# Kernel tuning notes

Measured on AMD Instinct MI355X. Metric: run time of the kernel, lower is better.

## Reference

```python
import jax, jax.numpy as jnp
import numpy as np

N_U, N_I, E = 100000, 100000, 600000
F_U, F_I, H, OUT = 96, 160, 128, 64
EPS = 1e-5


def _params(key):
    ks = jax.random.split(key, 20)
    n = lambda i, s: (jax.random.normal(ks[i], s, jnp.float32) * 0.05)
    p = {
        # lazy per-type input projections
        'Wp_u': n(0, (F_U, H)), 'bp_u': jnp.zeros((H,), jnp.float32),
        'Wp_i': n(1, (F_I, H)), 'bp_i': jnp.zeros((H,), jnp.float32),
        # layer 0 SAGE (in=H, out=H): lin_l (neighbors, bias), lin_r (root, no bias)
        'Wl0_ui': n(2, (H, H)), 'bl0_ui': jnp.zeros((H,), jnp.float32), 'Wr0_ui': n(3, (H, H)),
        'Wl0_iu': n(4, (H, H)), 'bl0_iu': jnp.zeros((H,), jnp.float32), 'Wr0_iu': n(5, (H, H)),
        'g0_u': jnp.ones((H,), jnp.float32), 'b0_u': jnp.zeros((H,), jnp.float32),
        'g0_i': jnp.ones((H,), jnp.float32), 'b0_i': jnp.zeros((H,), jnp.float32),
        # layer 1 SAGE (in=H, out=OUT)
        'Wl1_ui': n(6, (H, OUT)), 'bl1_ui': jnp.zeros((OUT,), jnp.float32), 'Wr1_ui': n(7, (H, OUT)),
        'Wl1_iu': n(8, (H, OUT)), 'bl1_iu': jnp.zeros((OUT,), jnp.float32), 'Wr1_iu': n(9, (H, OUT)),
        'g1_u': jnp.ones((OUT,), jnp.float32), 'b1_u': jnp.zeros((OUT,), jnp.float32),
        'g1_i': jnp.ones((OUT,), jnp.float32), 'b1_i': jnp.zeros((OUT,), jnp.float32),
    }
    return p


def setup_inputs() -> dict:
    key = jax.random.key(0)
    k0, k1, k2, k3, kp = jax.random.split(key, 5)
    inp = {
        'x_user': jax.random.normal(k0, (N_U, F_U), jnp.float32),
        'x_item': jax.random.normal(k1, (N_I, F_I), jnp.float32),
        'edge_ui': jax.random.randint(k2, (2, E), 0, N_U),  # row0: src user idx, row1: dst item idx
        'edge_iu': jax.random.randint(k3, (2, E), 0, N_I),  # row0: src item idx, row1: dst user idx
    }
    inp.update(_params(kp))
    return inp


def _seg_mean(x_src, src, dst, n_dst):
    # gather source features [E, C], scatter-mean into destinations [n_dst, C]
    msg = x_src[src]
    s = jax.ops.segment_sum(msg, dst, num_segments=n_dst)
    cnt = jax.ops.segment_sum(jnp.ones((dst.shape[0], 1), x_src.dtype), dst, num_segments=n_dst)
    return s / jnp.maximum(cnt, 1.0)


def _sage(x_src, x_dst, edge, Wl, bl, Wr, n_dst):
    agg = _seg_mean(x_src, edge[0], edge[1], n_dst)
    return agg @ Wl + bl + x_dst @ Wr


def _ln(h, g, b):
    m = jnp.mean(h, axis=-1, keepdims=True)
    v = jnp.mean(jnp.square(h - m), axis=-1, keepdims=True)
    return (h - m) * jax.lax.rsqrt(v + EPS) * g + b


def reference(x_user, x_item, edge_ui, edge_iu,
              Wp_u, bp_u, Wp_i, bp_i,
              Wl0_ui, bl0_ui, Wr0_ui, Wl0_iu, bl0_iu, Wr0_iu,
              g0_u, b0_u, g0_i, b0_i,
              Wl1_ui, bl1_ui, Wr1_ui, Wl1_iu, bl1_iu, Wr1_iu,
              g1_u, b1_u, g1_i, b1_i):
    # per-type input projection + ReLU
    h_u = jax.nn.relu(x_user @ Wp_u + bp_u)
    h_i = jax.nn.relu(x_item @ Wp_i + bp_i)
    # layer 0: HeteroConv(sum) of SAGEConv per edge type, then per-type LN + ReLU (dropout = eval identity)
    h_i1 = _sage(h_u, h_i, edge_ui, Wl0_ui, bl0_ui, Wr0_ui, N_I)
    h_u1 = _sage(h_i, h_u, edge_iu, Wl0_iu, bl0_iu, Wr0_iu, N_U)
    h_u1 = jax.nn.relu(_ln(h_u1, g0_u, b0_u))
    h_i1 = jax.nn.relu(_ln(h_i1, g0_i, b0_i))
    # layer 1 (final): SAGE -> LN, no ReLU/dropout
    h_i2 = _sage(h_u1, h_i1, edge_ui, Wl1_ui, bl1_ui, Wr1_ui, N_I)
    h_u2 = _sage(h_i1, h_u1, edge_iu, Wl1_iu, bl1_iu, Wr1_iu, N_U)
    h_u2 = _ln(h_u2, g1_u, b1_u)
    h_i2 = _ln(h_i2, g1_i, b1_i)
    return h_u2, h_i2
```

## Files before the change

kernel.cpp:

```cpp
#include <hip/hip_runtime.h>

typedef __attribute__((ext_vector_type(8))) __bf16 bf16x8;
typedef __attribute__((ext_vector_type(4))) float floatx4;
typedef __attribute__((ext_vector_type(8))) unsigned short ushort8v;
typedef __attribute__((ext_vector_type(4))) unsigned short ushort4v;

namespace {
constexpr int kNU = 100000, kNI = 100000, kE = 600000;
constexpr int kFU = 96, kFI = 160, kH = 128, kOUT = 64;
constexpr float kEPS = 1e-5f;
constexpr int kM = 32;
constexpr int kNCHUNK = 98;
constexpr int kNBLK = kNU / kM;
constexpr int kEB = (kE + 255) / 256;
constexpr int kPART = kNU / 8;
}

__device__ __forceinline__ unsigned short f2b(float f) {
  unsigned u = __builtin_bit_cast(unsigned, f);
  u += 0x7FFFu + ((u >> 16) & 1u);
  return (unsigned short)(u >> 16);
}
__device__ __forceinline__ float b2f(unsigned short h) {
  return __builtin_bit_cast(float, (unsigned)h << 16);
}
__device__ __forceinline__ void split3(float v, unsigned short& h,
                                       unsigned short& m, unsigned short& l) {
  h = f2b(v);
  const float r1 = v - b2f(h);
  m = f2b(r1);
  const float r2 = r1 - b2f(m);
  l = f2b(r2);
}
__device__ __forceinline__ void split2(float v, unsigned short& h,
                                       unsigned short& m) {
  h = f2b(v);
  m = f2b(v - b2f(h));
}
__device__ __forceinline__ bf16x8 ldb8(const unsigned short* p) {
  return __builtin_bit_cast(bf16x8, *(const ushort8v*)p);
}
__device__ __forceinline__ floatx4 mfma16(bf16x8 a, bf16x8 b, floatx4 c) {
  return __builtin_amdgcn_mfma_f32_16x16x32_bf16(a, b, c, 0, 0, 0);
}
__device__ __forceinline__ unsigned short* ab_ptr(unsigned short* base,
                                                  int plane, int r, int bo) {
  return (unsigned short*)((char*)base + plane * 8192 + r * 256 +
                           (bo ^ ((r & 7) << 4)));
}

struct WcvtArgs {
  const float* src[10];
  unsigned short* dh[10];
  unsigned short* dm[10];
  unsigned short* dl[10];
  int K[10], N[10];
};
__global__ __launch_bounds__(256) void wcvt(WcvtArgs a) {
  const int m = blockIdx.y;
  const int K = a.K[m], N = a.N[m];
  const int idx = blockIdx.x * 256 + threadIdx.x;
  if (idx < K * N) {
    const int n = idx / K, k = idx - n * K;
    unsigned short h, mm, l;
    split3(a.src[m][(size_t)k * N + n], h, mm, l);
    a.dh[m][idx] = h;
    a.dm[m][idx] = mm;
    a.dl[m][idx] = l;
  }
}

__global__ void zero_int(int* __restrict__ p, int n) {
  int i = blockIdx.x * blockDim.x + threadIdx.x;
  const int st = gridDim.x * blockDim.x;
  for (; i < n; i += st) p[i] = 0;
}

__global__ __launch_bounds__(1024) void scanA(const int* __restrict__ cnt_u,
                                              const int* __restrict__ cnt_i,
                                              int* ptr_u, int* ptr_i, int* tot) {
  __shared__ int sh[1024];
  const int dir = blockIdx.y;
  const int* cnt = dir ? cnt_i : cnt_u;
  int* ptr = dir ? ptr_i : ptr_u;
  const int t = threadIdx.x;
  const int i = blockIdx.x * 1024 + t;
  const int v = (i < kNU) ? cnt[i] : 0;
  sh[t] = v;
  __syncthreads();
  for (int o = 1; o < 1024; o <<= 1) {
    const int y = (t >= o) ? sh[t - o] : 0;
    __syncthreads();
    sh[t] += y;
    __syncthreads();
  }
  if (i < kNU) ptr[i] = sh[t] - v;
  if (t == 1023) tot[dir * 128 + blockIdx.x] = sh[1023];
}

__global__ __launch_bounds__(128) void scanB(int* tot) {
  __shared__ int sh[128];
  int* tp = tot + blockIdx.x * 128;
  const int t = threadIdx.x;
  const int v = (t < kNCHUNK) ? tp[t] : 0;
  sh[t] = v;
  __syncthreads();
  for (int o = 1; o < 128; o <<= 1) {
    const int y = (t >= o) ? sh[t - o] : 0;
    __syncthreads();
    sh[t] += y;
    __syncthreads();
  }
  if (t < kNCHUNK) tp[t] = sh[t] - v;
}

__global__ __launch_bounds__(1024) void scanC(int* ptr_u, int* ptr_i,
                                              const int* __restrict__ tot,
                                              int* cur_u, int* cur_i) {
  const int dir = blockIdx.y;
  int* ptr = dir ? ptr_i : ptr_u;
  int* cur = dir ? cur_i : cur_u;
  const int i = blockIdx.x * 1024 + threadIdx.x;
  if (i < kNU) {
    const int v = ptr[i] + tot[dir * 128 + blockIdx.x];
    ptr[i] = v;
    cur[i] = v;
  }
}

template <int F>
__device__ __forceinline__ void proj_body(
    const float* __restrict__ x, const unsigned short* __restrict__ Wh,
    const unsigned short* __restrict__ Wm, const unsigned short* __restrict__ Wl,
    const float* __restrict__ bias, float* __restrict__ out, int blk,
    unsigned short* sh) {
  constexpr int AS = F + 8, KC = F / 32;
  unsigned short* Ah = sh;
  unsigned short* Am = sh + kM * AS;
  unsigned short* Al = sh + 2 * kM * AS;
  const int tid = threadIdx.x;
  const size_t row0 = (size_t)blk * kM;
  for (int c = tid; c < kM * (F / 4); c += 256) {
    const int r = c / (F / 4), j = c % (F / 4);
    const float4 v = *(const float4*)&x[(row0 + r) * F + j * 4];
    const float* vv = &v.x;
    ushort4v h4, m4, l4;
#pragma unroll
    for (int u = 0; u < 4; ++u) {
      unsigned short th, tm, tl;
      split3(vv[u], th, tm, tl);
      h4[u] = th; m4[u] = tm; l4[u] = tl;
    }
    *(ushort4v*)&Ah[r * AS + j * 4] = h4;
    *(ushort4v*)&Am[r * AS + j * 4] = m4;
    *(ushort4v*)&Al[r * AS + j * 4] = l4;
  }
  const int lane = tid & 63, w = tid >> 6, q = lane >> 4, ln = lane & 15;
  floatx4 acc[2][2] = {}, accL[2][2] = {};
  __syncthreads();
#pragma unroll
  for (int kc = 0; kc < KC; ++kc) {
    bf16x8 bh[2], bm[2], bl_[2];
#pragma unroll
    for (int t = 0; t < 2; ++t) {
      const int off = (w * 32 + t * 16 + ln) * F + kc * 32 + q * 8;
      bh[t] = ldb8(&Wh[off]);
      bm[t] = ldb8(&Wm[off]);
      bl_[t] = ldb8(&Wl[off]);
    }
#pragma unroll
    for (int mt = 0; mt < 2; ++mt) {
      const int ro = mt * 16 + ln, co = kc * 32 + q * 8;
      const bf16x8 ah = ldb8(&Ah[ro * AS + co]);
      const bf16x8 am = ldb8(&Am[ro * AS + co]);
      const bf16x8 al = ldb8(&Al[ro * AS + co]);
#pragma unroll
      for (int t = 0; t < 2; ++t) {
        acc[mt][t] = mfma16(ah, bh[t], acc[mt][t]);
        floatx4 cl = accL[mt][t];
        cl = mfma16(ah, bm[t], cl);
        cl = mfma16(am, bh[t], cl);
        cl = mfma16(ah, bl_[t], cl);
        cl = mfma16(al, bh[t], cl);
        cl = mfma16(am, bm[t], cl);
        accL[mt][t] = cl;
      }
    }
  }
#pragma unroll
  for (int t = 0; t < 2; ++t) {
    const int col = w * 32 + t * 16 + ln;
    const float bv = bias[col];
#pragma unroll
    for (int mt = 0; mt < 2; ++mt)
#pragma unroll
      for (int r = 0; r < 4; ++r)
        out[(row0 + mt * 16 + q * 4 + r) * kH + col] =
            fmaxf((acc[mt][t][r] + accL[mt][t][r]) + bv, 0.f);
  }
}

__global__ __launch_bounds__(256, 4) void hist_proj(
    const int* __restrict__ eui, const int* __restrict__ eiu, int* cnt_i,
    int* cnt_u, const float* __restrict__ x,
    const unsigned short* __restrict__ Wh, const unsigned short* __restrict__ Wm,
    const unsigned short* __restrict__ Wl, const float* __restrict__ bias,
    float* __restrict__ out) {
  __shared__ __align__(16) unsigned short sh[3 * kM * (kFU + 8)];
  if (blockIdx.x < 8 * kEB) {
    const int part = blockIdx.x & 7, slice = blockIdx.x >> 3;
    const int e = slice * 256 + threadIdx.x;
    if (e < kE) {
      const int di = eui[kE + e];
      if (di / kPART == part) atomicAdd(&cnt_i[di], 1);
      const int du = eiu[kE + e];
      if (du / kPART == part) atomicAdd(&cnt_u[du], 1);
    }
  } else {
    proj_body<kFU>(x, Wh, Wm, Wl, bias, out, blockIdx.x - 8 * kEB, sh);
  }
}

__global__ __launch_bounds__(256, 4) void fill_proj(
    const int* __restrict__ eui, const int* __restrict__ eiu, int* cur_i,
    int* cur_u, int* __restrict__ col_ui, int* __restrict__ col_iu,
    const float* __restrict__ x, const unsigned short* __restrict__ Wh,
    const unsigned short* __restrict__ Wm, const unsigned short* __restrict__ Wl,
    const float* __restrict__ bias, float* __restrict__ out) {
  __shared__ __align__(16) unsigned short sh[3 * kM * (kFI + 8)];
  if (blockIdx.x < 8 * kEB) {
    const int part = blockIdx.x & 7, slice = blockIdx.x >> 3;
    const int e = slice * 256 + threadIdx.x;
    if (e < kE) {
      const int di = eui[kE + e];
      if (di / kPART == part) {
        const int p = atomicAdd(&cur_i[di], 1);
        col_ui[p] = eui[e];
      }
      const int du = eiu[kE + e];
      if (du / kPART == part) {
        const int p2 = atomicAdd(&cur_u[du], 1);
        col_iu[p2] = eiu[e];
      }
    }
  } else {
    proj_body<kFI>(x, Wh, Wm, Wl, bias, out, blockIdx.x - 8 * kEB, sh);
  }
}

struct AggArgs {
  const float* src[2];
  const int* ptr[2];
  const int* cur[2];
  const int* col[2];
  float* out[2];
};
template <int W>
__global__ __launch_bounds__(256) void agg2(AggArgs a) {
  const int dir = blockIdx.y;
  const int w = threadIdx.x >> 6, lane = threadIdx.x & 63;
  const int row = blockIdx.x * 4 + w;
  const float* __restrict__ feat = a.src[dir];
  const int* __restrict__ col = a.col[dir];
  const int beg = a.ptr[dir][row], end = a.cur[dir][row];
  const float inv = 1.0f / fmaxf((float)(end - beg), 1.0f);
  if (W == 128) {
    float s0 = 0.f, s1 = 0.f;
    for (int e = beg; e < end; e += 8) {
      const int n = end - e;
      float2 v[8];
#pragma unroll
      for (int j = 0; j < 8; ++j)
        if (j < n) v[j] = *(const float2*)&feat[(size_t)col[e + j] * 128 + lane * 2];
#pragma unroll
      for (int j = 0; j < 8; ++j)
        if (j < n) { s0 += v[j].x; s1 += v[j].y; }
    }
    float2 o;
    o.x = s0 * inv;
    o.y = s1 * inv;
    *(float2*)&a.out[dir][(size_t)row * 128 + lane * 2] = o;
  } else {
    float s = 0.f;
    for (int e = beg; e < end; e += 8) {
      const int n = end - e;
      float v[8];
#pragma unroll
      for (int j = 0; j < 8; ++j)
        if (j < n) v[j] = feat[(size_t)col[e + j] * 64 + lane];
#pragma unroll
      for (int j = 0; j < 8; ++j)
        if (j < n) s += v[j];
    }
    a.out[dir][(size_t)row * 64 + lane] = s * inv;
  }
}

struct FsArgs {
  const float* agg[2];
  const float* root[2];
  const unsigned short *WLh[2], *WLm[2];
  const unsigned short *WRh[2], *WRm[2];
  const float *bl[2], *g[2], *b[2];
  float* out[2];
};
__global__ __launch_bounds__(256, 5) void sage0(FsArgs a) {
  constexpr int NOUT = 128;
  __shared__ __align__(16) unsigned short Ab[4 * kM * kH];
  float* Cs = (float*)Ab;
  const int tid = threadIdx.x;
  const int dir = blockIdx.y;
  const size_t row0 = (size_t)blockIdx.x * kM;
  const float* __restrict__ agg = a.agg[dir];
  const float* __restrict__ root = a.root[dir];

  {
    float4 va[8];
#pragma unroll
    for (int k = 0; k < 8; ++k) {
      const int c = tid + k * 256;
      const int cc = c & 1023, r = cc >> 5, j = cc & 31;
      va[k] = *(const float4*)((k < 4 ? agg : root) + (row0 + r) * kH + j * 4);
    }
#pragma unroll
    for (int k = 0; k < 8; ++k) {
      const int c = tid + k * 256;
      const int mat = k >> 2, cc = c & 1023, r = cc >> 5, j = cc & 31;
      const float* vv = &va[k].x;
      ushort4v h4, m4;
#pragma unroll
      for (int u = 0; u < 4; ++u) {
        unsigned short th, tm;
        split2(vv[u], th, tm);
        h4[u] = th; m4[u] = tm;
      }
      *(ushort4v*)ab_ptr(Ab, mat * 2 + 0, r, j * 8) = h4;
      *(ushort4v*)ab_ptr(Ab, mat * 2 + 1, r, j * 8) = m4;
    }
  }

  const int lane = tid & 63, w = tid >> 6, q = lane >> 4, ln = lane & 15;
  floatx4 acc[2][2] = {}, accL[2][2] = {};
  const unsigned short* __restrict__ WLh = a.WLh[dir];
  const unsigned short* __restrict__ WLm = a.WLm[dir];
  const unsigned short* __restrict__ WRh = a.WRh[dir];
  const unsigned short* __restrict__ WRm = a.WRm[dir];
  __syncthreads();
#pragma unroll
  for (int kc = 0; kc < 4; ++kc) {
    bf16x8 BL[2][2], BR[2][2];
#pragma unroll
    for (int t = 0; t < 2; ++t) {
      const int off = (w * 32 + t * 16 + ln) * kH + kc * 32 + q * 8;
      BL[0][t] = ldb8(&WLh[off]);
      BL[1][t] = ldb8(&WLm[off]);
      BR[0][t] = ldb8(&WRh[off]);
      BR[1][t] = ldb8(&WRm[off]);
    }
#pragma unroll
    for (int mt = 0; mt < 2; ++mt) {
      const int ro = mt * 16 + ln, cob = kc * 64 + q * 16;
      const bf16x8 a1h = ldb8(ab_ptr(Ab, 0, ro, cob));
      const bf16x8 a1m = ldb8(ab_ptr(Ab, 1, ro, cob));
      const bf16x8 a2h = ldb8(ab_ptr(Ab, 2, ro, cob));
      const bf16x8 a2m = ldb8(ab_ptr(Ab, 3, ro, cob));
#pragma unroll
      for (int t = 0; t < 2; ++t) {
        floatx4 c = acc[mt][t];
        c = mfma16(a1h, BL[0][t], c);
        c = mfma16(a2h, BR[0][t], c);
        acc[mt][t] = c;
        floatx4 cl = accL[mt][t];
        cl = mfma16(a1h, BL[1][t], cl);
        cl = mfma16(a1m, BL[0][t], cl);
        cl = mfma16(a2h, BR[1][t], cl);
        cl = mfma16(a2m, BR[0][t], cl);
        accL[mt][t] = cl;
      }
    }
  }
  __syncthreads();
  const float* __restrict__ blv = a.bl[dir];
#pragma unroll
  for (int t = 0; t < 2; ++t) {
    const int colx = (w * 2 + t) * 16 + ln;
    const float bv = blv[colx];
#pragma unroll
    for (int mt = 0; mt < 2; ++mt)
#pragma unroll
      for (int r = 0; r < 4; ++r)
        Cs[(mt * 16 + q * 4 + r) * (NOUT + 1) + colx] =
            (acc[mt][t][r] + accL[mt][t][r]) + bv;
  }
  __syncthreads();
  const int r = tid >> 3, sub = tid & 7;
  const float* __restrict__ gg = a.g[dir];
  const float* __restrict__ bb = a.b[dir];
  float vals[16], s = 0.f;
#pragma unroll
  for (int j = 0; j < 16; ++j) {
    const float v = Cs[r * (NOUT + 1) + sub * 16 + j];
    vals[j] = v;
    s += v;
  }
#pragma unroll
  for (int o = 1; o < 8; o <<= 1) s += __shfl_xor(s, o, 64);
  const float mean = s * (1.0f / NOUT);
  float s2 = 0.f;
#pragma unroll
  for (int j = 0; j < 16; ++j) {
    const float d = vals[j] - mean;
    s2 += d * d;
  }
#pragma unroll
  for (int o = 1; o < 8; o <<= 1) s2 += __shfl_xor(s2, o, 64);
  const float rstd = rsqrtf(s2 * (1.0f / NOUT) + kEPS);
  float* op = a.out[dir] + (row0 + r) * NOUT + sub * 16;
#pragma unroll
  for (int j = 0; j < 16; j += 4) {
    float4 o4;
    float* oo = &o4.x;
#pragma unroll
    for (int jj = 0; jj < 4; ++jj)
      oo[jj] = fmaxf((vals[j + jj] - mean) * rstd * gg[sub * 16 + j + jj] +
                         bb[sub * 16 + j + jj],
                     0.f);
    *(float4*)&op[j] = o4;
  }
}

struct ZArgs {
  const float* src[2];
  const unsigned short *Bh[2], *Bm[2];
  float* out[2];
};
__global__ __launch_bounds__(256, 6) void zproj(ZArgs a) {
  __shared__ __align__(16) unsigned short Ab[2 * kM * kH];
  const int tid = threadIdx.x, dir = blockIdx.y;
  const size_t row0 = (size_t)blockIdx.x * kM;
  const float* __restrict__ src = a.src[dir];
  {
    float4 va[4];
#pragma unroll
    for (int k = 0; k < 4; ++k) {
      const int c = tid + k * 256, r = c >> 5, j = c & 31;
      va[k] = *(const float4*)&src[(row0 + r) * kH + j * 4];
    }
#pragma unroll
    for (int k = 0; k < 4; ++k) {
      const int c = tid + k * 256, r = c >> 5, j = c & 31;
      const float* vv = &va[k].x;
      ushort4v h4, m4;
#pragma unroll
      for (int u = 0; u < 4; ++u) {
        unsigned short th, tm;
        split2(vv[u], th, tm);
        h4[u] = th; m4[u] = tm;
      }
      *(ushort4v*)ab_ptr(Ab, 0, r, j * 8) = h4;
      *(ushort4v*)ab_ptr(Ab, 1, r, j * 8) = m4;
    }
  }
  const int lane = tid & 63, w = tid >> 6, q = lane >> 4, ln = lane & 15;
  const unsigned short* __restrict__ Bh = a.Bh[dir];
  const unsigned short* __restrict__ Bm = a.Bm[dir];
  floatx4 acc[2] = {}, accL[2] = {};
  __syncthreads();
#pragma unroll
  for (int kc = 0; kc < 4; ++kc) {
    const int off = (w * 16 + ln) * kH + kc * 32 + q * 8;
    const bf16x8 bh = ldb8(&Bh[off]);
    const bf16x8 bm = ldb8(&Bm[off]);
#pragma unroll
    for (int mt = 0; mt < 2; ++mt) {
      const int ro = mt * 16 + ln, cob = kc * 64 + q * 16;
      const bf16x8 ah = ldb8(ab_ptr(Ab, 0, ro, cob));
      const bf16x8 am = ldb8(ab_ptr(Ab, 1, ro, cob));
      acc[mt] = mfma16(ah, bh, acc[mt]);
      floatx4 cl = accL[mt];
      cl = mfma16(ah, bm, cl);
      cl = mfma16(am, bh, cl);
      accL[mt] = cl;
    }
  }
  float* __restrict__ out = a.out[dir];
  const int col = w * 16 + ln;
#pragma unroll
  for (int mt = 0; mt < 2; ++mt)
#pragma unroll
    for (int r = 0; r < 4; ++r)
      out[(row0 + mt * 16 + q * 4 + r) * kOUT + col] =
          acc[mt][r] + accL[mt][r];
}

struct S1Args {
  const float* root[2];
  const float* aggz[2];
  const unsigned short *Bh[2], *Bm[2];
  const float *bl[2], *g[2], *b[2];
  float* out[2];
};
__global__ __launch_bounds__(256, 6) void sage1(S1Args a) {
  constexpr int NOUT = kOUT;
  __shared__ __align__(16) unsigned short Ab[2 * kM * kH];
  float* Cs = (float*)Ab;
  const int tid = threadIdx.x, dir = blockIdx.y;
  const size_t row0 = (size_t)blockIdx.x * kM;
  const float* __restrict__ root = a.root[dir];
  {
    float4 va[4];
#pragma unroll
    for (int k = 0; k < 4; ++k) {
      const int c = tid + k * 256, r = c >> 5, j = c & 31;
      va[k] = *(const float4*)&root[(row0 + r) * kH + j * 4];
    }
#pragma unroll
    for (int k = 0; k < 4; ++k) {
      const int c = tid + k * 256, r = c >> 5, j = c & 31;
      const float* vv = &va[k].x;
      ushort4v h4, m4;
#pragma unroll
      for (int u = 0; u < 4; ++u) {
        unsigned short th, tm;
        split2(vv[u], th, tm);
        h4[u] = th; m4[u] = tm;
      }
      *(ushort4v*)ab_ptr(Ab, 0, r, j * 8) = h4;
      *(ushort4v*)ab_ptr(Ab, 1, r, j * 8) = m4;
    }
  }
  const int lane = tid & 63, w = tid >> 6, q = lane >> 4, ln = lane & 15;
  const unsigned short* __restrict__ Bh = a.Bh[dir];
  const unsigned short* __restrict__ Bm = a.Bm[dir];
  floatx4 acc[2] = {}, accL[2] = {};
  __syncthreads();
#pragma unroll
  for (int kc = 0; kc < 4; ++kc) {
    const int off = (w * 16 + ln) * kH + kc * 32 + q * 8;
    const bf16x8 bh = ldb8(&Bh[off]);
    const bf16x8 bm = ldb8(&Bm[off]);
#pragma unroll
    for (int mt = 0; mt < 2; ++mt) {
      const int ro = mt * 16 + ln, cob = kc * 64 + q * 16;
      const bf16x8 ah = ldb8(ab_ptr(Ab, 0, ro, cob));
      const bf16x8 am = ldb8(ab_ptr(Ab, 1, ro, cob));
      acc[mt] = mfma16(ah, bh, acc[mt]);
      floatx4 cl = accL[mt];
      cl = mfma16(ah, bm, cl);
      cl = mfma16(am, bh, cl);
      accL[mt] = cl;
    }
  }
  __syncthreads();
  const float* __restrict__ blv = a.bl[dir];
  {
    const int col = w * 16 + ln;
    const float bv = blv[col];
#pragma unroll
    for (int mt = 0; mt < 2; ++mt)
#pragma unroll
      for (int r = 0; r < 4; ++r)
        Cs[(mt * 16 + q * 4 + r) * (NOUT + 1) + col] =
            (acc[mt][r] + accL[mt][r]) + bv;
  }
  __syncthreads();
  const int r = tid >> 3, sub = tid & 7;
  const float* __restrict__ az = a.aggz[dir];
  const float* __restrict__ gg = a.g[dir];
  const float* __restrict__ bb = a.b[dir];
  const float4 az0 = *(const float4*)&az[(row0 + r) * NOUT + sub * 8];
  const float4 az1 = *(const float4*)&az[(row0 + r) * NOUT + sub * 8 + 4];
  float vals[8], s = 0.f;
#pragma unroll
  for (int j = 0; j < 8; ++j) {
    const float v = Cs[r * (NOUT + 1) + sub * 8 + j] +
                    (j < 4 ? (&az0.x)[j] : (&az1.x)[j - 4]);
    vals[j] = v;
    s += v;
  }
#pragma unroll
  for (int o = 1; o < 8; o <<= 1) s += __shfl_xor(s, o, 64);
  const float mean = s * (1.0f / NOUT);
  float s2 = 0.f;
#pragma unroll
  for (int j = 0; j < 8; ++j) {
    const float d = vals[j] - mean;
    s2 += d * d;
  }
#pragma unroll
  for (int o = 1; o < 8; o <<= 1) s2 += __shfl_xor(s2, o, 64);
  const float rstd = rsqrtf(s2 * (1.0f / NOUT) + kEPS);
  float* op = a.out[dir] + (row0 + r) * NOUT + sub * 8;
#pragma unroll
  for (int j = 0; j < 8; j += 4) {
    float4 o4;
    float* oo = &o4.x;
#pragma unroll
    for (int jj = 0; jj < 4; ++jj)
      oo[jj] = (vals[j + jj] - mean) * rstd * gg[sub * 8 + j + jj] +
               bb[sub * 8 + j + jj];
    *(float4*)&op[j] = o4;
  }
}

extern "C" void kernel_launch(void* const* d_in, const int* in_sizes, int n_in,
                              void* d_out, int out_size, void* d_ws, size_t ws_size,
                              hipStream_t stream) {
  (void)in_sizes; (void)n_in; (void)out_size; (void)ws_size;
  const float* x_u    = (const float*)d_in[0];
  const float* x_i    = (const float*)d_in[1];
  const int*   e_ui   = (const int*)d_in[2];
  const int*   e_iu   = (const int*)d_in[3];
  const float* Wp_u   = (const float*)d_in[4];
  const float* bp_u   = (const float*)d_in[5];
  const float* Wp_i   = (const float*)d_in[6];
  const float* bp_i   = (const float*)d_in[7];
  const float* Wl0_ui = (const float*)d_in[8];
  const float* bl0_ui = (const float*)d_in[9];
  const float* Wr0_ui = (const float*)d_in[10];
  const float* Wl0_iu = (const float*)d_in[11];
  const float* bl0_iu = (const float*)d_in[12];
  const float* Wr0_iu = (const float*)d_in[13];
  const float* g0_u   = (const float*)d_in[14];
  const float* b0_u   = (const float*)d_in[15];
  const float* g0_i   = (const float*)d_in[16];
  const float* b0_i   = (const float*)d_in[17];
  const float* Wl1_ui = (const float*)d_in[18];
  const float* bl1_ui = (const float*)d_in[19];
  const float* Wr1_ui = (const float*)d_in[20];
  const float* Wl1_iu = (const float*)d_in[21];
  const float* bl1_iu = (const float*)d_in[22];
  const float* Wr1_iu = (const float*)d_in[23];
  const float* g1_u   = (const float*)d_in[24];
  const float* b1_u   = (const float*)d_in[25];
  const float* g1_i   = (const float*)d_in[26];
  const float* b1_i   = (const float*)d_in[27];

  float* pf = (float*)d_ws;
  const size_t NH = (size_t)kNU * kH;
  float* hu0 = pf;
  float* hi0 = pf + NH;
  float* b2  = pf + 2 * NH;
  float* b3  = pf + 3 * NH;
  float* Zu = hu0;
  float* Zi = hu0 + (size_t)kNU * kOUT;
  float* aggzI = hi0;
  float* aggzU = hi0 + (size_t)kNU * kOUT;
  unsigned short* wh = (unsigned short*)(pf + 4 * NH);
  unsigned short* wm = wh + 131072;
  unsigned short* wl = wm + 131072;
  int* pi = (int*)(wl + 131072);
  int* cnt_u = pi; pi += kNU;
  int* cnt_i = pi; pi += kNU;
  int* ptr_u = pi; pi += kNU;
  int* ptr_i = pi; pi += kNU;
  int* cur_u = pi; pi += kNU;
  int* cur_i = pi; pi += kNU;
  int* tot   = pi; pi += 2 * 128;
  int* col_ui = pi; pi += kE;
  int* col_iu = pi; pi += kE;

  const int oPu = 0, oPi = 12288, o0Lui = 32768, o0Rui = 49152,
            o0Liu = 65536, o0Riu = 81920, o1Lui = 98304, o1Rui = 106496,
            o1Liu = 114688, o1Riu = 122880;

  float* out_u = (float*)d_out;
  float* out_i = out_u + (size_t)kNU * kOUT;

  WcvtArgs wa;
  const float* wsrc[10] = {Wp_u, Wp_i, Wl0_ui, Wr0_ui, Wl0_iu, Wr0_iu,
                           Wl1_ui, Wr1_ui, Wl1_iu, Wr1_iu};
  const int woff[10] = {oPu, oPi, o0Lui, o0Rui, o0Liu, o0Riu,
                        o1Lui, o1Rui, o1Liu, o1Riu};
  const int wK[10] = {kFU, kFI, kH, kH, kH, kH, kH, kH, kH, kH};
  const int wN[10] = {kH, kH, kH, kH, kH, kH, kOUT, kOUT, kOUT, kOUT};
  for (int i = 0; i < 10; ++i) {
    wa.src[i] = wsrc[i];
    wa.dh[i] = wh + woff[i];
    wa.dm[i] = wm + woff[i];
    wa.dl[i] = wl + woff[i];
    wa.K[i] = wK[i];
    wa.N[i] = wN[i];
  }
  wcvt<<<dim3(80, 10), 256, 0, stream>>>(wa);

  zero_int<<<256, 256, 0, stream>>>(cnt_u, 2 * kNU);
  hist_proj<<<8 * kEB + kNBLK, 256, 0, stream>>>(e_ui, e_iu, cnt_i, cnt_u, x_u,
                                                 wh + oPu, wm + oPu, wl + oPu,
                                                 bp_u, hu0);
  scanA<<<dim3(kNCHUNK, 2), 1024, 0, stream>>>(cnt_u, cnt_i, ptr_u, ptr_i, tot);
  scanB<<<2, 128, 0, stream>>>(tot);
  scanC<<<dim3(kNCHUNK, 2), 1024, 0, stream>>>(ptr_u, ptr_i, tot, cur_u, cur_i);
  fill_proj<<<8 * kEB + kNBLK, 256, 0, stream>>>(e_ui, e_iu, cur_i, cur_u,
                                                 col_ui, col_iu, x_i, wh + oPi,
                                                 wm + oPi, wl + oPi, bp_i, hi0);

  AggArgs g0;
  g0.src[0] = hu0; g0.ptr[0] = ptr_i; g0.cur[0] = cur_i; g0.col[0] = col_ui;
  g0.out[0] = b2;
  g0.src[1] = hi0; g0.ptr[1] = ptr_u; g0.cur[1] = cur_u; g0.col[1] = col_iu;
  g0.out[1] = b3;
  agg2<kH><<<dim3(kNU / 4, 2), 256, 0, stream>>>(g0);

  FsArgs a0;
  a0.agg[0] = b2; a0.root[0] = hi0;
  a0.WLh[0] = wh + o0Lui; a0.WLm[0] = wm + o0Lui;
  a0.WRh[0] = wh + o0Rui; a0.WRm[0] = wm + o0Rui;
  a0.bl[0] = bl0_ui; a0.g[0] = g0_i; a0.b[0] = b0_i; a0.out[0] = b2;
  a0.agg[1] = b3; a0.root[1] = hu0;
  a0.WLh[1] = wh + o0Liu; a0.WLm[1] = wm + o0Liu;
  a0.WRh[1] = wh + o0Riu; a0.WRm[1] = wm + o0Riu;
  a0.bl[1] = bl0_iu; a0.g[1] = g0_u; a0.b[1] = b0_u; a0.out[1] = b3;
  sage0<<<dim3(kNBLK, 2), 256, 0, stream>>>(a0);

  ZArgs zp;
  zp.src[0] = b3;
  zp.Bh[0] = wh + o1Lui; zp.Bm[0] = wm + o1Lui;
  zp.out[0] = Zu;
  zp.src[1] = b2;
  zp.Bh[1] = wh + o1Liu; zp.Bm[1] = wm + o1Liu;
  zp.out[1] = Zi;
  zproj<<<dim3(kNBLK, 2), 256, 0, stream>>>(zp);

  AggArgs g1;
  g1.src[0] = Zu; g1.ptr[0] = ptr_i; g1.cur[0] = cur_i; g1.col[0] = col_ui;
  g1.out[0] = aggzI;
  g1.src[1] = Zi; g1.ptr[1] = ptr_u; g1.cur[1] = cur_u; g1.col[1] = col_iu;
  g1.out[1] = aggzU;
  agg2<kOUT><<<dim3(kNU / 4, 2), 256, 0, stream>>>(g1);

  S1Args s1;
  s1.root[0] = b2; s1.aggz[0] = aggzI;
  s1.Bh[0] = wh + o1Rui; s1.Bm[0] = wm + o1Rui;
  s1.bl[0] = bl1_ui; s1.g[0] = g1_i; s1.b[0] = b1_i; s1.out[0] = out_i;
  s1.root[1] = b3; s1.aggz[1] = aggzU;
  s1.Bh[1] = wh + o1Riu; s1.Bm[1] = wm + o1Riu;
  s1.bl[1] = bl1_iu; s1.g[1] = g1_u; s1.b[1] = b1_u; s1.out[1] = out_u;
  sage1<<<dim3(kNBLK, 2), 256, 0, stream>>>(s1);
}
```

Baseline: 765.4 us.

## Fuse layer-1 neighbor projection into sage0 and stage inputs via direct global-to-LDS loads

```diff
diff --git a/kernel.cpp b/kernel.cpp
--- a/kernel.cpp
+++ b/kernel.cpp
@@ -43,10 +43,31 @@
 __device__ __forceinline__ floatx4 mfma16(bf16x8 a, bf16x8 b, floatx4 c) {
   return __builtin_amdgcn_mfma_f32_16x16x32_bf16(a, b, c, 0, 0, 0);
 }
-__device__ __forceinline__ unsigned short* ab_ptr(unsigned short* base,
-                                                  int plane, int r, int bo) {
+__device__ __forceinline__ unsigned short* ab_ptr(void* base, int plane, int r,
+                                                  int bo) {
   return (unsigned short*)((char*)base + plane * 8192 + r * 256 +
                            (bo ^ ((r & 7) << 4)));
+}
+__device__ __forceinline__ void gload_lds16(const void* g, void* l) {
+  __builtin_amdgcn_global_load_lds(
+      (const __attribute__((address_space(1))) void*)g,
+      (__attribute__((address_space(3))) void*)l, 16, 0, 0);
+}
+__device__ __forceinline__ void split8(const float4& x, const float4& y,
+                                       bf16x8& h8, bf16x8& m8) {
+  ushort8v h, m;
+  const float* p0 = &x.x;
+  const float* p1 = &y.x;
+#pragma unroll
+  for (int u = 0; u < 4; ++u) {
+    unsigned short th, tm;
+    split2(p0[u], th, tm);
+    h[u] = th; m[u] = tm;
+    split2(p1[u], th, tm);
+    h[4 + u] = th; m[4 + u] = tm;
+  }
+  h8 = __builtin_bit_cast(bf16x8, h);
+  m8 = __builtin_bit_cast(bf16x8, m);
 }
 
 struct WcvtArgs {
@@ -268,10 +289,15 @@
     float s0 = 0.f, s1 = 0.f;
     for (int e = beg; e < end; e += 8) {
       const int n = end - e;
+      int cidx[8];
+#pragma unroll
+      for (int j = 0; j < 8; ++j) cidx[j] = col[(j < n) ? (e + j) : e];
+      __builtin_amdgcn_sched_barrier(0);
       float2 v[8];
 #pragma unroll
       for (int j = 0; j < 8; ++j)
-        if (j < n) v[j] = *(const float2*)&feat[(size_t)col[e + j] * 128 + lane * 2];
+        if (j < n) v[j] = *(const float2*)&feat[(size_t)cidx[j] * 128 + lane * 2];
+      __builtin_amdgcn_sched_barrier(0);
 #pragma unroll
       for (int j = 0; j < 8; ++j)
         if (j < n) { s0 += v[j].x; s1 += v[j].y; }
@@ -284,10 +310,15 @@
     float s = 0.f;
     for (int e = beg; e < end; e += 8) {
       const int n = end - e;
+      int cidx[8];
+#pragma unroll
+      for (int j = 0; j < 8; ++j) cidx[j] = col[(j < n) ? (e + j) : e];
+      __builtin_amdgcn_sched_barrier(0);
       float v[8];
 #pragma unroll
       for (int j = 0; j < 8; ++j)
-        if (j < n) v[j] = feat[(size_t)col[e + j] * 64 + lane];
+        if (j < n) v[j] = feat[(size_t)cidx[j] * 64 + lane];
+      __builtin_amdgcn_sched_barrier(0);
 #pragma unroll
       for (int j = 0; j < 8; ++j)
         if (j < n) s += v[j];
@@ -301,50 +332,40 @@
   const float* root[2];
   const unsigned short *WLh[2], *WLm[2];
   const unsigned short *WRh[2], *WRm[2];
+  const unsigned short *ZBh[2], *ZBm[2];
   const float *bl[2], *g[2], *b[2];
   float* out[2];
+  float* zout[2];
 };
-__global__ __launch_bounds__(256, 5) void sage0(FsArgs a) {
+__global__ __launch_bounds__(256, 4) void sage0(FsArgs a) {
   constexpr int NOUT = 128;
-  __shared__ __align__(16) unsigned short Ab[4 * kM * kH];
-  float* Cs = (float*)Ab;
+  __shared__ __align__(16) char Lds[32768];
+  float* Cs = (float*)Lds;
   const int tid = threadIdx.x;
   const int dir = blockIdx.y;
   const size_t row0 = (size_t)blockIdx.x * kM;
   const float* __restrict__ agg = a.agg[dir];
   const float* __restrict__ root = a.root[dir];
-
-  {
-    float4 va[8];
-#pragma unroll
-    for (int k = 0; k < 8; ++k) {
-      const int c = tid + k * 256;
-      const int cc = c & 1023, r = cc >> 5, j = cc & 31;
-      va[k] = *(const float4*)((k < 4 ? agg : root) + (row0 + r) * kH + j * 4);
-    }
-#pragma unroll
-    for (int k = 0; k < 8; ++k) {
-      const int c = tid + k * 256;
-      const int mat = k >> 2, cc = c & 1023, r = cc >> 5, j = cc & 31;
-      const float* vv = &va[k].x;
-      ushort4v h4, m4;
-#pragma unroll
-      for (int u = 0; u < 4; ++u) {
-        unsigned short th, tm;
-        split2(vv[u], th, tm);
-        h4[u] = th; m4[u] = tm;
-      }
-      *(ushort4v*)ab_ptr(Ab, mat * 2 + 0, r, j * 8) = h4;
-      *(ushort4v*)ab_ptr(Ab, mat * 2 + 1, r, j * 8) = m4;
-    }
-  }
-
-  const int lane = tid & 63, w = tid >> 6, q = lane >> 4, ln = lane & 15;
-  floatx4 acc[2][2] = {}, accL[2][2] = {};
   const unsigned short* __restrict__ WLh = a.WLh[dir];
   const unsigned short* __restrict__ WLm = a.WLm[dir];
   const unsigned short* __restrict__ WRh = a.WRh[dir];
   const unsigned short* __restrict__ WRm = a.WRm[dir];
+  const int lane = tid & 63, w = tid >> 6, q = lane >> 4, ln = lane & 15;
+
+  {
+    const char* g0 = (const char*)agg + row0 * 512;
+    const char* g1 = (const char*)root + row0 * 512;
+#pragma unroll
+    for (int c = 0; c < 4; ++c) {
+      const int sbase = (w * 4 + c) * 1024;
+      const int s = sbase + lane * 16;
+      const int soff = s ^ (((s >> 9) & 7) << 4);
+      gload_lds16(g0 + soff, Lds + sbase);
+      gload_lds16(g1 + soff, Lds + 16384 + sbase);
+    }
+  }
+
+  floatx4 acc[2][2] = {}, accL[2][2] = {};
   __syncthreads();
 #pragma unroll
   for (int kc = 0; kc < 4; ++kc) {
@@ -359,11 +380,16 @@
     }
 #pragma unroll
     for (int mt = 0; mt < 2; ++mt) {
-      const int ro = mt * 16 + ln, cob = kc * 64 + q * 16;
-      const bf16x8 a1h = ldb8(ab_ptr(Ab, 0, ro, cob));
-      const bf16x8 a1m = ldb8(ab_ptr(Ab, 1, ro, cob));
-      const bf16x8 a2h = ldb8(ab_ptr(Ab, 2, ro, cob));
-      const bf16x8 a2m = ldb8(ab_ptr(Ab, 3, ro, cob));
+      const int ro = mt * 16 + ln;
+      const int lb = ro * 512 + kc * 128 + q * 32;
+      const int xr = (ro & 7) << 4;
+      const float4 fa0 = *(const float4*)(Lds + (lb ^ xr));
+      const float4 fa1 = *(const float4*)(Lds + ((lb + 16) ^ xr));
+      const float4 fr0 = *(const float4*)(Lds + 16384 + (lb ^ xr));
+      const float4 fr1 = *(const float4*)(Lds + 16384 + ((lb + 16) ^ xr));
+      bf16x8 a1h, a1m, a2h, a2m;
+      split8(fa0, fa1, a1h, a1m);
+      split8(fr0, fr1, a2h, a2m);
 #pragma unroll
       for (int t = 0; t < 2; ++t) {
         floatx4 c = acc[mt][t];
@@ -416,81 +442,64 @@
   for (int o = 1; o < 8; o <<= 1) s2 += __shfl_xor(s2, o, 64);
   const float rstd = rsqrtf(s2 * (1.0f / NOUT) + kEPS);
   float* op = a.out[dir] + (row0 + r) * NOUT + sub * 16;
+  float zv[16];
 #pragma unroll
   for (int j = 0; j < 16; j += 4) {
     float4 o4;
     float* oo = &o4.x;
 #pragma unroll
-    for (int jj = 0; jj < 4; ++jj)
-      oo[jj] = fmaxf((vals[j + jj] - mean) * rstd * gg[sub * 16 + j + jj] +
-                         bb[sub * 16 + j + jj],
-                     0.f);
+    for (int jj = 0; jj < 4; ++jj) {
+      const float hv = fmaxf((vals[j + jj] - mean) * rstd * gg[sub * 16 + j + jj] +
+                                 bb[sub * 16 + j + jj],
+                             0.f);
+      oo[jj] = hv;
+      zv[j + jj] = hv;
+    }
     *(float4*)&op[j] = o4;
   }
-}
-
-struct ZArgs {
-  const float* src[2];
-  const unsigned short *Bh[2], *Bm[2];
-  float* out[2];
-};
-__global__ __launch_bounds__(256, 6) void zproj(ZArgs a) {
-  __shared__ __align__(16) unsigned short Ab[2 * kM * kH];
-  const int tid = threadIdx.x, dir = blockIdx.y;
-  const size_t row0 = (size_t)blockIdx.x * kM;
-  const float* __restrict__ src = a.src[dir];
-  {
-    float4 va[4];
-#pragma unroll
-    for (int k = 0; k < 4; ++k) {
-      const int c = tid + k * 256, r = c >> 5, j = c & 31;
-      va[k] = *(const float4*)&src[(row0 + r) * kH + j * 4];
-    }
-#pragma unroll
-    for (int k = 0; k < 4; ++k) {
-      const int c = tid + k * 256, r = c >> 5, j = c & 31;
-      const float* vv = &va[k].x;
-      ushort4v h4, m4;
-#pragma unroll
-      for (int u = 0; u < 4; ++u) {
-        unsigned short th, tm;
-        split2(vv[u], th, tm);
-        h4[u] = th; m4[u] = tm;
-      }
-      *(ushort4v*)ab_ptr(Ab, 0, r, j * 8) = h4;
-      *(ushort4v*)ab_ptr(Ab, 1, r, j * 8) = m4;
-    }
-  }
-  const int lane = tid & 63, w = tid >> 6, q = lane >> 4, ln = lane & 15;
-  const unsigned short* __restrict__ Bh = a.Bh[dir];
-  const unsigned short* __restrict__ Bm = a.Bm[dir];
-  floatx4 acc[2] = {}, accL[2] = {};
+  __syncthreads();
+#pragma unroll
+  for (int j = 0; j < 16; j += 8) {
+    ushort8v h8, m8;
+#pragma unroll
+    for (int u = 0; u < 8; ++u) {
+      unsigned short th, tm;
+      split2(zv[j + u], th, tm);
+      h8[u] = th; m8[u] = tm;
+    }
+    const int bo = sub * 32 + j * 2;
+    *(ushort8v*)ab_ptr(Lds, 0, r, bo) = h8;
+    *(ushort8v*)ab_ptr(Lds, 1, r, bo) = m8;
+  }
+  const unsigned short* __restrict__ ZBh = a.ZBh[dir];
+  const unsigned short* __restrict__ ZBm = a.ZBm[dir];
+  floatx4 zacc[2] = {}, zaccL[2] = {};
   __syncthreads();
 #pragma unroll
   for (int kc = 0; kc < 4; ++kc) {
     const int off = (w * 16 + ln) * kH + kc * 32 + q * 8;
-    const bf16x8 bh = ldb8(&Bh[off]);
-    const bf16x8 bm = ldb8(&Bm[off]);
+    const bf16x8 zbh = ldb8(&ZBh[off]);
+    const bf16x8 zbm = ldb8(&ZBm[off]);
 #pragma unroll
     for (int mt = 0; mt < 2; ++mt) {
       const int ro = mt * 16 + ln, cob = kc * 64 + q * 16;
-      const bf16x8 ah = ldb8(ab_ptr(Ab, 0, ro, cob));
-      const bf16x8 am = ldb8(ab_ptr(Ab, 1, ro, cob));
-      acc[mt] = mfma16(ah, bh, acc[mt]);
-      floatx4 cl = accL[mt];
-      cl = mfma16(ah, bm, cl);
-      cl = mfma16(am, bh, cl);
-      accL[mt] = cl;
-    }
-  }
-  float* __restrict__ out = a.out[dir];
-  const int col = w * 16 + ln;
+      const bf16x8 ah = ldb8(ab_ptr(Lds, 0, ro, cob));
+      const bf16x8 am = ldb8(ab_ptr(Lds, 1, ro, cob));
+      zacc[mt] = mfma16(ah, zbh, zacc[mt]);
+      floatx4 cl = zaccL[mt];
+      cl = mfma16(ah, zbm, cl);
+      cl = mfma16(am, zbh, cl);
+      zaccL[mt] = cl;
+    }
+  }
+  float* __restrict__ zo = a.zout[dir];
+  const int zcol = w * 16 + ln;
 #pragma unroll
   for (int mt = 0; mt < 2; ++mt)
 #pragma unroll
-    for (int r = 0; r < 4; ++r)
-      out[(row0 + mt * 16 + q * 4 + r) * kOUT + col] =
-          acc[mt][r] + accL[mt][r];
+    for (int rr = 0; rr < 4; ++rr)
+      zo[(row0 + mt * 16 + q * 4 + rr) * kOUT + zcol] =
+          zacc[mt][rr] + zaccL[mt][rr];
 }
 
 struct S1Args {
@@ -500,54 +509,58 @@
   const float *bl[2], *g[2], *b[2];
   float* out[2];
 };
-__global__ __launch_bounds__(256, 6) void sage1(S1Args a) {
+__global__ __launch_bounds__(256, 5) void sage1(S1Args a) {
   constexpr int NOUT = kOUT;
   __shared__ __align__(16) unsigned short Ab[2 * kM * kH];
   float* Cs = (float*)Ab;
   const int tid = threadIdx.x, dir = blockIdx.y;
   const size_t row0 = (size_t)blockIdx.x * kM;
   const float* __restrict__ root = a.root[dir];
-  {
-    float4 va[4];
-#pragma unroll
-    for (int k = 0; k < 4; ++k) {
-      const int c = tid + k * 256, r = c >> 5, j = c & 31;
-      va[k] = *(const float4*)&root[(row0 + r) * kH + j * 4];
-    }
-#pragma unroll
-    for (int k = 0; k < 4; ++k) {
-      const int c = tid + k * 256, r = c >> 5, j = c & 31;
-      const float* vv = &va[k].x;
-      ushort4v h4, m4;
-#pragma unroll
-      for (int u = 0; u < 4; ++u) {
-        unsigned short th, tm;
-        split2(vv[u], th, tm);
-        h4[u] = th; m4[u] = tm;
-      }
-      *(ushort4v*)ab_ptr(Ab, 0, r, j * 8) = h4;
-      *(ushort4v*)ab_ptr(Ab, 1, r, j * 8) = m4;
-    }
-  }
-  const int lane = tid & 63, w = tid >> 6, q = lane >> 4, ln = lane & 15;
   const unsigned short* __restrict__ Bh = a.Bh[dir];
   const unsigned short* __restrict__ Bm = a.Bm[dir];
-  floatx4 acc[2] = {}, accL[2] = {};
-  __syncthreads();
+  const int lane = tid & 63, w = tid >> 6, q = lane >> 4, ln = lane & 15;
+
+  float4 va[4];
+#pragma unroll
+  for (int k = 0; k < 4; ++k) {
+    const int c = tid + k * 256, r = c >> 5, j = c & 31;
+    va[k] = *(const float4*)&root[(row0 + r) * kH + j * 4];
+  }
+  bf16x8 Bh4[4], Bm4[4];
 #pragma unroll
   for (int kc = 0; kc < 4; ++kc) {
     const int off = (w * 16 + ln) * kH + kc * 32 + q * 8;
-    const bf16x8 bh = ldb8(&Bh[off]);
-    const bf16x8 bm = ldb8(&Bm[off]);
+    Bh4[kc] = ldb8(&Bh[off]);
+    Bm4[kc] = ldb8(&Bm[off]);
+  }
+  __builtin_amdgcn_sched_barrier(0);
+#pragma unroll
+  for (int k = 0; k < 4; ++k) {
+    const int c = tid + k * 256, r = c >> 5, j = c & 31;
+    const float* vv = &va[k].x;
+    ushort4v h4, m4;
+#pragma unroll
+    for (int u = 0; u < 4; ++u) {
+      unsigned short th, tm;
+      split2(vv[u], th, tm);
+      h4[u] = th; m4[u] = tm;
+    }
+    *(ushort4v*)ab_ptr(Ab, 0, r, j * 8) = h4;
+    *(ushort4v*)ab_ptr(Ab, 1, r, j * 8) = m4;
+  }
+  floatx4 acc[2] = {}, accL[2] = {};
+  __syncthreads();
+#pragma unroll
+  for (int kc = 0; kc < 4; ++kc) {
 #pragma unroll
     for (int mt = 0; mt < 2; ++mt) {
       const int ro = mt * 16 + ln, cob = kc * 64 + q * 16;
       const bf16x8 ah = ldb8(ab_ptr(Ab, 0, ro, cob));
       const bf16x8 am = ldb8(ab_ptr(Ab, 1, ro, cob));
-      acc[mt] = mfma16(ah, bh, acc[mt]);
+      acc[mt] = mfma16(ah, Bh4[kc], acc[mt]);
       floatx4 cl = accL[mt];
-      cl = mfma16(ah, bm, cl);
-      cl = mfma16(am, bh, cl);
+      cl = mfma16(ah, Bm4[kc], cl);
+      cl = mfma16(am, Bh4[kc], cl);
       accL[mt] = cl;
     }
   }
@@ -642,8 +655,6 @@
   float* hi0 = pf + NH;
   float* b2  = pf + 2 * NH;
   float* b3  = pf + 3 * NH;
-  float* Zu = hu0;
-  float* Zi = hu0 + (size_t)kNU * kOUT;
   float* aggzI = hi0;
   float* aggzU = hi0 + (size_t)kNU * kOUT;
   unsigned short* wh = (unsigned short*)(pf + 4 * NH);
@@ -666,6 +677,8 @@
 
   float* out_u = (float*)d_out;
   float* out_i = out_u + (size_t)kNU * kOUT;
+  float* Zu = out_u;
+  float* Zi = out_i;
 
   WcvtArgs wa;
   const float* wsrc[10] = {Wp_u, Wp_i, Wl0_ui, Wr0_ui, Wl0_iu, Wr0_iu,
@@ -706,21 +719,18 @@
   a0.agg[0] = b2; a0.root[0] = hi0;
   a0.WLh[0] = wh + o0Lui; a0.WLm[0] = wm + o0Lui;
   a0.WRh[0] = wh + o0Rui; a0.WRm[0] = wm + o0Rui;
-  a0.bl[0] = bl0_ui; a0.g[0] = g0_i; a0.b[0] = b0_i; a0.out[0] = b2;
+  a0.ZBh[0] = wh + o1Liu; a0.ZBm[0] = wm + o1Liu;
+  a0.bl[0] = bl0_ui; a0.g[0] = g0_i; a0.b[0] = b0_i;
+  a0.out[0] = b2;
+  a0.zout[0] = Zi;
   a0.agg[1] = b3; a0.root[1] = hu0;
   a0.WLh[1] = wh + o0Liu; a0.WLm[1] = wm + o0Liu;
   a0.WRh[1] = wh + o0Riu; a0.WRm[1] = wm + o0Riu;
-  a0.bl[1] = bl0_iu; a0.g[1] = g0_u; a0.b[1] = b0_u; a0.out[1] = b3;
+  a0.ZBh[1] = wh + o1Lui; a0.ZBm[1] = wm + o1Lui;
+  a0.bl[1] = bl0_iu; a0.g[1] = g0_u; a0.b[1] = b0_u;
+  a0.out[1] = b3;
+  a0.zout[1] = Zu;
   sage0<<<dim3(kNBLK, 2), 256, 0, stream>>>(a0);
-
-  ZArgs zp;
-  zp.src[0] = b3;
-  zp.Bh[0] = wh + o1Lui; zp.Bm[0] = wm + o1Lui;
-  zp.out[0] = Zu;
-  zp.src[1] = b2;
-  zp.Bh[1] = wh + o1Liu; zp.Bm[1] = wm + o1Liu;
-  zp.out[1] = Zi;
-  zproj<<<dim3(kNBLK, 2), 256, 0, stream>>>(zp);
 
   AggArgs g1;
   g1.src[0] = Zu; g1.ptr[0] = ptr_i; g1.cur[0] = cur_i; g1.col[0] = col_ui;
```

New measurement: 713.3 us. -6.8%, faster.
